# Performance work log

Measured on AMD Instinct MI355X. Metric: run time of the kernel, lower is better.

Reference implementation:

```python
import jax, jax.numpy as jnp
import numpy as np

B, T, N, F_IN = 2, 4, 1024, 256
H, N_HIDDEN = 8, 128
SLOPE = 0.2
NEG_INF = -9e16


def setup_inputs() -> dict:
    key = jax.random.key(0)
    k1, k2, k3, k4 = jax.random.split(key, 4)
    h = jax.random.normal(k1, (B, T, N, F_IN), dtype=jnp.float32)
    adj_mat = jax.random.randint(k2, (N, N), 0, 2, dtype=jnp.int32)
    W = jax.random.normal(k3, (F_IN, H * N_HIDDEN), dtype=jnp.float32) * 0.05
    a = jax.random.normal(k4, (H, 2 * N_HIDDEN, 1), dtype=jnp.float32) * 0.05
    return {"h": h, "adj_mat": adj_mat, "W": W, "a": a}


def reference(h, adj_mat, W, a):
    b, t, n, _ = h.shape
    # linear transform: [B,T,N,F_in] @ [F_in, H*nh] -> [B,T,N,H*nh]
    ht = jnp.einsum('btjs,sh->btjh', h, W)
    # dropout is identity in eval mode
    ht = ht.reshape(b, t, n, H, N_HIDDEN).transpose(0, 1, 3, 2, 4)  # [B,T,H,N,nh]
    # additive attention scores
    a_src = a[:, :N_HIDDEN, :]   # [H, nh, 1]
    a_tgt = a[:, N_HIDDEN:, :]   # [H, nh, 1]
    src = jnp.einsum('bthnd,hdo->bthno', ht, a_src)  # [B,T,H,N,1]
    tgt = jnp.einsum('bthnd,hdo->bthno', ht, a_tgt)  # [B,T,H,N,1]
    e = src + jnp.swapaxes(tgt, -1, -2)              # [B,T,H,N,N]
    e = jnp.where(e >= 0, e, SLOPE * e)              # LeakyReLU
    e = jnp.where(adj_mat > 0, e, jnp.float32(NEG_INF))
    attention = jax.nn.softmax(e, axis=-1)
    # weighted aggregation: [B,T,H,N,N] @ [B,T,H,N,nh]
    h_prime = jnp.einsum('bthij,bthjd->bthid', attention, ht)
    # concat=False branch: mean over dim 0 (batch), as in the source
    return h_prime.mean(axis=0)  # [T,H,N,nh]
```

## Files before the change

kernel.cpp:

```cpp
#include <hip/hip_runtime.h>
#include <cstddef>
#include <cstdint>

#define B_ 2
#define T_ 4
#define N_ 1024
#define FIN_ 256
#define H_ 8
#define D_ 128
#define L2E_ 1.4426950408889634f

typedef __attribute__((ext_vector_type(8))) short short8;
typedef __attribute__((ext_vector_type(4))) float f32x4;
typedef __attribute__((ext_vector_type(2))) float f32x2;

#define MFMA16(A, B, C) __builtin_amdgcn_mfma_f32_16x16x32_bf16((A), (B), (C), 0, 0, 0)

__device__ __forceinline__ unsigned short f2bf(float f) {
    uint32_t u = __float_as_uint(f);
    uint32_t r = (u + 0x7fffu + ((u >> 16) & 1u)) >> 16;
    return (unsigned short)r;
}

__device__ __forceinline__ uint32_t cvt_pk_bf16(float lo, float hi) {
    uint32_t r;
    asm volatile("v_cvt_pk_bf16_f32 %0, %1, %2" : "=v"(r) : "v"(lo), "v"(hi));
    return r;
}

__device__ __forceinline__ float fexp2(float x) {
#if __has_builtin(__builtin_amdgcn_exp2f)
    return __builtin_amdgcn_exp2f(x);
#else
    float r;
    asm("v_exp_f32 %0, %1" : "=v"(r) : "v"(x));
    return r;
#endif
}

__device__ __forceinline__ void load_lds16(const unsigned short* g, unsigned short* l) {
    __builtin_amdgcn_global_load_lds(
        (const __attribute__((address_space(1))) uint32_t*)g,
        (__attribute__((address_space(3))) uint32_t*)l, 16, 0, 0);
}

__global__ __launch_bounds__(256) void k_prep(const int* __restrict__ adj,
                                              const float* __restrict__ W,
                                              const float* __restrict__ a,
                                              unsigned short* __restrict__ Wt_bf,
                                              uint32_t* __restrict__ adjm,
                                              float* __restrict__ wa) {
    __shared__ float wl[64][68];
    const int bid = blockIdx.x, tid = threadIdx.x;
    if (bid < 512) {
        const int w0 = (bid * 256 + tid) * 4;
        const int4 p0 = *(const int4*)(adj + (size_t)w0 * 2);
        const int4 p1 = *(const int4*)(adj + (size_t)w0 * 2 + 4);
        uint4 m;
        m.x = (p0.x > 0 ? 0xFFFFu : 0u) | (p0.y > 0 ? 0xFFFF0000u : 0u);
        m.y = (p0.z > 0 ? 0xFFFFu : 0u) | (p0.w > 0 ? 0xFFFF0000u : 0u);
        m.z = (p1.x > 0 ? 0xFFFFu : 0u) | (p1.y > 0 ? 0xFFFF0000u : 0u);
        m.w = (p1.z > 0 ? 0xFFFFu : 0u) | (p1.w > 0 ? 0xFFFF0000u : 0u);
        *(uint4*)(adjm + w0) = m;
    } else if (bid < 576) {
        const int tb  = bid - 512;
        const int hk0 = (tb >> 2) * 64;
        const int s0  = (tb & 3) * 64;
        {
            const int r  = tid >> 2;
            const int c0 = (tid & 3) * 16;
            #pragma unroll
            for (int k = 0; k < 4; ++k)
                *(float4*)&wl[r][c0 + k * 4] =
                    *(const float4*)(W + (size_t)(s0 + r) * (H_ * D_) + hk0 + c0 + k * 4);
        }
        __syncthreads();
        {
            const int r2 = tid >> 2;
            const int c2 = (tid & 3) * 16;
            unsigned short ob[16];
            #pragma unroll
            for (int k = 0; k < 16; ++k) ob[k] = f2bf(wl[c2 + k][r2]);
            unsigned short* dst = Wt_bf + (size_t)(hk0 + r2) * FIN_ + s0 + c2;
            *(uint4*)(dst)     = *(uint4*)&ob[0];
            *(uint4*)(dst + 8) = *(uint4*)&ob[8];
        }
    } else {
        const int o    = (bid - 576) * 256 + tid;
        const int head = o >> 9;
        const int st   = (o >> 8) & 1;
        const int s    = o & 255;
        const float* wr = W + (size_t)s * (H_ * D_) + head * D_;
        const float* ar = a + head * 256 + st * 128;
        float sum = 0.f;
        #pragma unroll
        for (int d = 0; d < 128; d += 4) {
            const float4 wv = *(const float4*)(wr + d);
            const float4 av = *(const float4*)(ar + d);
            sum += wv.x * av.x + wv.y * av.y + wv.z * av.z + wv.w * av.w;
        }
        wa[s * 16 + head * 2 + st] = sum;
    }
}

__global__ __launch_bounds__(256, 2) void k_gemm_sp(const float* __restrict__ h,
                                                    const unsigned short* __restrict__ Wt_bf,
                                                    const float* __restrict__ wa,
                                                    unsigned short* __restrict__ htT,
                                                    float* __restrict__ s1,
                                                    float* __restrict__ t1) {
    __shared__ __align__(16) char smem[24576];
    const int bid = blockIdx.x, tid = threadIdx.x;
    if (bid < 1024) {
        unsigned short* a_lds = (unsigned short*)smem;
        unsigned short* b_lds = (unsigned short*)(smem + 16384);
        const int xcd  = bid & 7;
        const int slot = bid >> 3;
        const int gid  = xcd * 8 + (slot >> 4);
        const int bt   = gid >> 3;
        const int n0   = (gid & 7) * 128;
        const int hk0  = (slot & 15) * 64;
        const int w = tid >> 6, lane = tid & 63;
        const int row16 = lane & 15, kgrp = lane >> 4;
        const int kswz = (kgrp ^ ((row16 >> 1) & 3)) * 8;
        const int ar  = tid >> 1;
        const int akh = tid & 1;
        const int asub = ar >> 4, arow = ar & 15;
        const int ax = (arow >> 1) & 3;
        const int aslot0 = ((akh * 2) ^ ax) * 8;
        const int aslot1 = ((akh * 2 + 1) ^ ax) * 8;
        const float* ga = h + ((size_t)bt * N_ + n0 + ar) * FIN_ + akh * 16;
        unsigned short* aw_ = a_lds + asub * 512 + arow * 32;
        const int brow = lane >> 2;
        const int bsb  = (lane & 3) ^ ((lane >> 3) & 3);
        const unsigned short* gb = Wt_bf + (size_t)(hk0 + w * 16 + brow) * FIN_ + bsb * 8;
        unsigned short* bw_ = b_lds + w * 512 + (size_t)lane * 8;

        float4 rf0, rf1, rf2, rf3;

#define LOADA(KS) {                                                            \
        const float* g = ga + (KS) * 32;                                       \
        rf0 = *(const float4*)(g);      rf1 = *(const float4*)(g + 4);         \
        rf2 = *(const float4*)(g + 8);  rf3 = *(const float4*)(g + 12); }

#define WRITEA(BUF) {                                                          \
        uint4 o0, o1;                                                          \
        o0.x = cvt_pk_bf16(rf0.x, rf0.y); o0.y = cvt_pk_bf16(rf0.z, rf0.w);    \
        o0.z = cvt_pk_bf16(rf1.x, rf1.y); o0.w = cvt_pk_bf16(rf1.z, rf1.w);    \
        o1.x = cvt_pk_bf16(rf2.x, rf2.y); o1.y = cvt_pk_bf16(rf2.z, rf2.w);    \
        o1.z = cvt_pk_bf16(rf3.x, rf3.y); o1.w = cvt_pk_bf16(rf3.z, rf3.w);    \
        unsigned short* ad = aw_ + (BUF) * 4096;                               \
        *(uint4*)(ad + aslot0) = o0;                                           \
        *(uint4*)(ad + aslot1) = o1; }

#define COMPK(BUF) {                                                           \
        const unsigned short* ab = a_lds + (BUF) * 4096;                       \
        const short8 bfv = *(const short8*)(b_lds + (BUF) * 2048 + w * 512 + row16 * 32 + kswz); \
        _Pragma("unroll")                                                      \
        for (int nt = 0; nt < 8; ++nt) {                                       \
            const short8 afv = *(const short8*)(ab + nt * 512 + row16 * 32 + kswz); \
            acc[nt] = MFMA16(afv, bfv, acc[nt]);                               \
        } }

        f32x4 acc[8];
        #pragma unroll
        for (int nt = 0; nt < 8; ++nt) acc[nt] = (f32x4){0.f, 0.f, 0.f, 0.f};

        LOADA(0)
        WRITEA(0)
        load_lds16(gb, bw_);
        LOADA(1)
        asm volatile("s_waitcnt vmcnt(4) lgkmcnt(0)" ::: "memory");
        __builtin_amdgcn_s_barrier();

        for (int ks = 0; ks < 8; ++ks) {
            const int cur = ks & 1;
            WRITEA(cur ^ 1)
            load_lds16(gb + ((ks + 1) & 7) * 32, bw_ + (cur ^ 1) * 2048);
            LOADA((ks + 2) & 7)
            COMPK(cur)
            asm volatile("s_waitcnt vmcnt(4) lgkmcnt(0)" ::: "memory");
            __builtin_amdgcn_s_barrier();
        }
#undef LOADA
#undef WRITEA
#undef COMPK
        const int hk   = hk0 + w * 16 + row16;
        const int head = hk >> 7;
        const int d    = hk & 127;
        unsigned short* ob = htT + ((size_t)(bt * H_ + head) * D_ + d) * N_;
        #pragma unroll
        for (int nt = 0; nt < 8; ++nt) {
            ushort4 v;
            v.x = f2bf(acc[nt][0]); v.y = f2bf(acc[nt][1]);
            v.z = f2bf(acc[nt][2]); v.w = f2bf(acc[nt][3]);
            *(ushort4*)(ob + n0 + nt * 16 + kgrp * 4) = v;
        }
    } else {
        float (*was)[16] = (float(*)[16])smem;
        {
            const int f = tid * 16;
            #pragma unroll
            for (int k = 0; k < 4; ++k)
                *(float4*)&was[f >> 4][k * 4] = *(const float4*)(wa + f + k * 4);
        }
        __syncthreads();
        const int r = tid >> 2, q = tid & 3;
        const int R = (bid - 1024) * 64 + r;
        const float* hrow = h + (size_t)R * FIN_ + q * 64;
        float acc[16];
        #pragma unroll
        for (int o = 0; o < 16; ++o) acc[o] = 0.f;
        for (int k = 0; k < 64; k += 4) {
            const float4 hv = *(const float4*)(hrow + k);
            const int s = q * 64 + k;
            #pragma unroll
            for (int kk = 0; kk < 4; ++kk) {
                const float hs = (kk == 0) ? hv.x : (kk == 1) ? hv.y : (kk == 2) ? hv.z : hv.w;
                #pragma unroll
                for (int o = 0; o < 16; ++o) acc[o] += hs * was[s + kk][o];
            }
        }
        #pragma unroll
        for (int o = 0; o < 16; ++o) {
            acc[o] += __shfl_xor(acc[o], 1);
            acc[o] += __shfl_xor(acc[o], 2);
        }
        const int bt = R >> 10, n = R & 1023;
        #pragma unroll
        for (int k = 0; k < 4; ++k) {
            const int o = q * 4 + k;
            const int head = o >> 1;
            const size_t idx = ((size_t)(bt * H_ + head)) * N_ + n;
            const float v = acc[o] * L2E_;
            if (o & 1) t1[idx] = v;
            else       s1[idx] = v;
        }
    }
}

struct SC {
    float4 a1l, a1h;
    uint4  m4A, m4B;
};

__global__ __launch_bounds__(256, 2) void k_attn(const unsigned short* __restrict__ htT,
                                                 const float* __restrict__ s1,
                                                 const float* __restrict__ t1,
                                                 const uint32_t* __restrict__ adjm,
                                                 float* __restrict__ out) {
    __shared__ __align__(16) char smem[65536];
    unsigned short* stg = (unsigned short*)smem;
    const int xcd  = blockIdx.x & 7;
    const int slot = blockIdx.x >> 3;
    const int th   = xcd * 4 + (slot >> 4);
    const int i0   = (slot & 15) * 64;
    const int tid = threadIdx.x;
    const int w = tid >> 6, lane = tid & 63;
    const int b = w & 1, isub = w >> 1;
    const int row16 = lane & 15, kgrp = lane >> 4, jrel = kgrp * 8;
    const int kswz = (kgrp ^ ((row16 >> 1) & 3)) * 8;
    const int bth = b * (T_ * H_) + th;
    const int iA  = i0 + isub * 32 + row16;
    const int iB  = iA + 16;
    const float s1A = s1[(size_t)bth * N_ + iA];
    const float s1B = s1[(size_t)bth * N_ + iB];
    const f32x2 s1A2 = {s1A, s1A}, s1B2 = {s1B, s1B};
    const f32x2 c02  = {0.2f, 0.2f};
    const float* t1b = t1 + (size_t)bth * N_;
    const uint32_t* amA = adjm + (size_t)iA * (N_ / 2);
    const uint32_t* amB = adjm + (size_t)iB * (N_ / 2);

    const int sb  = w >> 1;
    const int sd0 = (w & 1) * 64 + (lane >> 2);
    const int sj  = ((lane & 3) ^ ((lane >> 3) & 3)) * 8;
    const unsigned short* gstg = htT + ((size_t)(sb * (T_ * H_) + th) * D_ + sd0) * N_ + sj;
    unsigned short* lstg = stg + (size_t)w * 2048 + (size_t)lane * 8;

#define STAGE(BUF, T32) {                                        \
        const unsigned short* gs = gstg + (size_t)(T32) * 32;    \
        unsigned short* ls = lstg + (BUF) * 8192;                \
        load_lds16(gs,           ls);                            \
        load_lds16(gs + 16 * N_, ls + 512);                      \
        load_lds16(gs + 32 * N_, ls + 1024);                     \
        load_lds16(gs + 48 * N_, ls + 1536); }

#define LOADSC(S, T32) {                                         \
        S.a1l = *(const float4*)(t1b + (T32) * 32 + jrel);       \
        S.a1h = *(const float4*)(t1b + (T32) * 32 + jrel + 4);   \
        S.m4A = *(const uint4*)(amA + (T32) * 16 + kgrp * 4);    \
        S.m4B = *(const uint4*)(amB + (T32) * 16 + kgrp * 4); }

    f32x4 accA[8], accB[8];
    #pragma unroll
    for (int nt = 0; nt < 8; ++nt) {
        accA[nt] = (f32x4){0.f, 0.f, 0.f, 0.f};
        accB[nt] = (f32x4){0.f, 0.f, 0.f, 0.f};
    }
    f32x4 daccA = (f32x4){0.f, 0.f, 0.f, 0.f};
    f32x4 daccB = (f32x4){0.f, 0.f, 0.f, 0.f};
    short8 ones8;
    {
        const short ov = (row16 == 0) ? (short)0x3F80 : (short)0;
        #pragma unroll
        for (int e = 0; e < 8; ++e) ones8[e] = ov;
    }
    const unsigned short* rdbase = stg + b * 4096 + row16 * 32 + kswz;

    SC scA, scB;

#define SUBP(BUFIDX, SCS, TNEXT)                                               \
    {                                                                          \
        const f32x2 tq[4] = {{SCS.a1l.x, SCS.a1l.y}, {SCS.a1l.z, SCS.a1l.w},   \
                             {SCS.a1h.x, SCS.a1h.y}, {SCS.a1h.z, SCS.a1h.w}};  \
        const uint32_t mAw[4] = {SCS.m4A.x, SCS.m4A.y, SCS.m4A.z, SCS.m4A.w};  \
        const uint32_t mBw[4] = {SCS.m4B.x, SCS.m4B.y, SCS.m4B.z, SCS.m4B.w};  \
        short8 afA, afB;                                                       \
        _Pragma("unroll")                                                      \
        for (int p = 0; p < 4; ++p) {                                          \
            const f32x2 eA  = s1A2 + tq[p];                                    \
            const f32x2 eB  = s1B2 + tq[p];                                    \
            const f32x2 eA2 = eA * c02;                                        \
            const f32x2 eB2 = eB * c02;                                        \
            const float wA0 = fexp2(fmaxf(eA[0], eA2[0]));                     \
            const float wA1 = fexp2(fmaxf(eA[1], eA2[1]));                     \
            const float wB0 = fexp2(fmaxf(eB[0], eB2[0]));                     \
            const float wB1 = fexp2(fmaxf(eB[1], eB2[1]));                     \
            ((uint32_t*)&afA)[p] = cvt_pk_bf16(wA0, wA1) & mAw[p];             \
            ((uint32_t*)&afB)[p] = cvt_pk_bf16(wB0, wB1) & mBw[p];             \
        }                                                                      \
        LOADSC(SCS, (TNEXT))                                                   \
        const unsigned short* rb = rdbase + (BUFIDX) * 8192;                   \
        short8 bfr[8];                                                         \
        _Pragma("unroll")                                                      \
        for (int nt = 0; nt < 8; ++nt) bfr[nt] = *(const short8*)(rb + nt * 512); \
        _Pragma("unroll")                                                      \
        for (int nt = 0; nt < 8; ++nt) {                                       \
            accA[nt] = MFMA16(afA, bfr[nt], accA[nt]);                         \
            accB[nt] = MFMA16(afB, bfr[nt], accB[nt]);                         \
        }                                                                      \
        daccA = MFMA16(afA, ones8, daccA);                                     \
        daccB = MFMA16(afB, ones8, daccB);                                     \
    }

    STAGE(0, 0)
    STAGE(1, 1)
    LOADSC(scA, 0)
    LOADSC(scB, 1)

    for (int T = 0; T < 16; ++T) {
        const int pair  = T & 1;
        const int npair = pair ^ 1;
        asm volatile("s_waitcnt vmcnt(8)" ::: "memory");
        __builtin_amdgcn_s_barrier();
        asm volatile("" ::: "memory");
        STAGE(npair * 2,     (2 * T + 2) & 31)
        STAGE(npair * 2 + 1, (2 * T + 3) & 31)
        SUBP(pair * 2,     scA, (2 * T + 2) & 31)
        SUBP(pair * 2 + 1, scB, (2 * T + 3) & 31)
    }
#undef SUBP
#undef LOADSC
#undef STAGE

    __syncthreads();

    float ivA[4], ivB[4];
    #pragma unroll
    for (int r = 0; r < 4; ++r) {
        ivA[r] = __shfl(1.0f / daccA[r], kgrp * 16);
        ivB[r] = __shfl(1.0f / daccB[r], kgrp * 16);
    }

    float* comb = (float*)smem;
    if (b == 1) {
        #pragma unroll
        for (int nt = 0; nt < 8; ++nt)
            #pragma unroll
            for (int r = 0; r < 4; ++r) {
                const int il = isub * 32 + kgrp * 4 + r;
                const int d  = nt * 16 + row16;
                comb[il * 128 + d]        = accA[nt][r] * ivA[r];
                comb[(il + 16) * 128 + d] = accB[nt][r] * ivB[r];
            }
    }
    __syncthreads();
    if (b == 0) {
        #pragma unroll
        for (int nt = 0; nt < 8; ++nt)
            #pragma unroll
            for (int r = 0; r < 4; ++r) {
                const int il = isub * 32 + kgrp * 4 + r;
                const int d  = nt * 16 + row16;
                out[((size_t)th * N_ + i0 + il) * D_ + d] =
                    0.5f * (accA[nt][r] * ivA[r] + comb[il * 128 + d]);
                out[((size_t)th * N_ + i0 + il + 16) * D_ + d] =
                    0.5f * (accB[nt][r] * ivB[r] + comb[(il + 16) * 128 + d]);
            }
    }
}

extern "C" void kernel_launch(void* const* d_in, const int* in_sizes, int n_in,
                              void* d_out, int out_size, void* d_ws, size_t ws_size,
                              hipStream_t stream) {
    const float* h   = (const float*)d_in[0];
    const int*   adj = (const int*)d_in[1];
    const float* W   = (const float*)d_in[2];
    const float* a   = (const float*)d_in[3];
    float* out = (float*)d_out;

    char* p = (char*)d_ws;
    unsigned short* htT = (unsigned short*)p;  p += (size_t)B_ * T_ * H_ * D_ * N_ * 2;
    float* s1 = (float*)p;                     p += (size_t)B_ * T_ * H_ * N_ * 4;
    float* t1 = (float*)p;                     p += (size_t)B_ * T_ * H_ * N_ * 4;
    uint32_t* adjm = (uint32_t*)p;             p += (size_t)N_ * N_ / 2 * 4;
    unsigned short* Wt_bf = (unsigned short*)p;p += (size_t)(H_ * D_) * FIN_ * 2;
    float* wa = (float*)p;

    k_prep<<<dim3(592), dim3(256), 0, stream>>>(adj, W, a, Wt_bf, adjm, wa);
    k_gemm_sp<<<dim3(1152), dim3(256), 0, stream>>>(h, Wt_bf, wa, htT, s1, t1);
    k_attn<<<dim3(512), dim3(256), 0, stream>>>(htT, s1, t1, adjm, out);
}
```

Measured before the change: 73.20 us.

## Move adjacency mask packing into GEMM kernel and make attention staging per-wave

```diff
diff --git a/kernel.cpp b/kernel.cpp
--- a/kernel.cpp
+++ b/kernel.cpp
@@ -44,26 +44,14 @@
         (__attribute__((address_space(3))) uint32_t*)l, 16, 0, 0);
 }
 
-__global__ __launch_bounds__(256) void k_prep(const int* __restrict__ adj,
-                                              const float* __restrict__ W,
+__global__ __launch_bounds__(256) void k_prep(const float* __restrict__ W,
                                               const float* __restrict__ a,
                                               unsigned short* __restrict__ Wt_bf,
-                                              uint32_t* __restrict__ adjm,
                                               float* __restrict__ wa) {
     __shared__ float wl[64][68];
     const int bid = blockIdx.x, tid = threadIdx.x;
-    if (bid < 512) {
-        const int w0 = (bid * 256 + tid) * 4;
-        const int4 p0 = *(const int4*)(adj + (size_t)w0 * 2);
-        const int4 p1 = *(const int4*)(adj + (size_t)w0 * 2 + 4);
-        uint4 m;
-        m.x = (p0.x > 0 ? 0xFFFFu : 0u) | (p0.y > 0 ? 0xFFFF0000u : 0u);
-        m.y = (p0.z > 0 ? 0xFFFFu : 0u) | (p0.w > 0 ? 0xFFFF0000u : 0u);
-        m.z = (p1.x > 0 ? 0xFFFFu : 0u) | (p1.y > 0 ? 0xFFFF0000u : 0u);
-        m.w = (p1.z > 0 ? 0xFFFFu : 0u) | (p1.w > 0 ? 0xFFFF0000u : 0u);
-        *(uint4*)(adjm + w0) = m;
-    } else if (bid < 576) {
-        const int tb  = bid - 512;
+    if (bid < 64) {
+        const int tb  = bid;
         const int hk0 = (tb >> 2) * 64;
         const int s0  = (tb & 3) * 64;
         {
@@ -86,7 +74,7 @@
             *(uint4*)(dst + 8) = *(uint4*)&ob[8];
         }
     } else {
-        const int o    = (bid - 576) * 256 + tid;
+        const int o    = (bid - 64) * 256 + tid;
         const int head = o >> 9;
         const int st   = (o >> 8) & 1;
         const int s    = o & 255;
@@ -106,9 +94,11 @@
 __global__ __launch_bounds__(256, 2) void k_gemm_sp(const float* __restrict__ h,
                                                     const unsigned short* __restrict__ Wt_bf,
                                                     const float* __restrict__ wa,
+                                                    const int* __restrict__ adj,
                                                     unsigned short* __restrict__ htT,
                                                     float* __restrict__ s1,
-                                                    float* __restrict__ t1) {
+                                                    float* __restrict__ t1,
+                                                    uint32_t* __restrict__ adjm) {
     __shared__ __align__(16) char smem[24576];
     const int bid = blockIdx.x, tid = threadIdx.x;
     if (bid < 1024) {
@@ -196,7 +186,7 @@
             v.z = f2bf(acc[nt][2]); v.w = f2bf(acc[nt][3]);
             *(ushort4*)(ob + n0 + nt * 16 + kgrp * 4) = v;
         }
-    } else {
+    } else if (bid < 1152) {
         float (*was)[16] = (float(*)[16])smem;
         {
             const int f = tid * 16;
@@ -236,6 +226,16 @@
             if (o & 1) t1[idx] = v;
             else       s1[idx] = v;
         }
+    } else {
+        const int w0 = ((bid - 1152) * 256 + tid) * 4;
+        const int4 p0 = *(const int4*)(adj + (size_t)w0 * 2);
+        const int4 p1 = *(const int4*)(adj + (size_t)w0 * 2 + 4);
+        uint4 m;
+        m.x = (p0.x > 0 ? 0xFFFFu : 0u) | (p0.y > 0 ? 0xFFFF0000u : 0u);
+        m.y = (p0.z > 0 ? 0xFFFFu : 0u) | (p0.w > 0 ? 0xFFFF0000u : 0u);
+        m.z = (p1.x > 0 ? 0xFFFFu : 0u) | (p1.y > 0 ? 0xFFFF0000u : 0u);
+        m.w = (p1.z > 0 ? 0xFFFFu : 0u) | (p1.w > 0 ? 0xFFFF0000u : 0u);
+        *(uint4*)(adjm + w0) = m;
     }
 }
 
@@ -271,19 +271,22 @@
     const uint32_t* amA = adjm + (size_t)iA * (N_ / 2);
     const uint32_t* amB = adjm + (size_t)iB * (N_ / 2);
 
-    const int sb  = w >> 1;
-    const int sd0 = (w & 1) * 64 + (lane >> 2);
-    const int sj  = ((lane & 3) ^ ((lane >> 3) & 3)) * 8;
-    const unsigned short* gstg = htT + ((size_t)(sb * (T_ * H_) + th) * D_ + sd0) * N_ + sj;
-    unsigned short* lstg = stg + (size_t)w * 2048 + (size_t)lane * 8;
+    const int sd0 = lane >> 2;
+    const int sj  = ((lane & 3) ^ ((sd0 >> 1) & 3)) * 8;
+    const unsigned short* gstg = htT + ((size_t)bth * D_ + sd0) * N_ + sj;
+    unsigned short* lstg = stg + (size_t)w * 8192 + (size_t)lane * 8;
 
 #define STAGE(BUF, T32) {                                        \
         const unsigned short* gs = gstg + (size_t)(T32) * 32;    \
-        unsigned short* ls = lstg + (BUF) * 8192;                \
-        load_lds16(gs,           ls);                            \
-        load_lds16(gs + 16 * N_, ls + 512);                      \
-        load_lds16(gs + 32 * N_, ls + 1024);                     \
-        load_lds16(gs + 48 * N_, ls + 1536); }
+        unsigned short* ls = lstg + (BUF) * 4096;                \
+        load_lds16(gs,            ls);                           \
+        load_lds16(gs + 16 * N_,  ls + 512);                     \
+        load_lds16(gs + 32 * N_,  ls + 1024);                    \
+        load_lds16(gs + 48 * N_,  ls + 1536);                    \
+        load_lds16(gs + 64 * N_,  ls + 2048);                    \
+        load_lds16(gs + 80 * N_,  ls + 2560);                    \
+        load_lds16(gs + 96 * N_,  ls + 3072);                    \
+        load_lds16(gs + 112 * N_, ls + 3584); }
 
 #define LOADSC(S, T32) {                                         \
         S.a1l = *(const float4*)(t1b + (T32) * 32 + jrel);       \
@@ -305,16 +308,16 @@
         #pragma unroll
         for (int e = 0; e < 8; ++e) ones8[e] = ov;
     }
-    const unsigned short* rdbase = stg + b * 4096 + row16 * 32 + kswz;
-
-    SC scA, scB;
-
-#define SUBP(BUFIDX, SCS, TNEXT)                                               \
+    const unsigned short* rdbase = stg + (size_t)w * 8192 + row16 * 32 + kswz;
+
+    SC sc;
+
+#define SUBP(BUFIDX, TNEXT)                                                    \
     {                                                                          \
-        const f32x2 tq[4] = {{SCS.a1l.x, SCS.a1l.y}, {SCS.a1l.z, SCS.a1l.w},   \
-                             {SCS.a1h.x, SCS.a1h.y}, {SCS.a1h.z, SCS.a1h.w}};  \
-        const uint32_t mAw[4] = {SCS.m4A.x, SCS.m4A.y, SCS.m4A.z, SCS.m4A.w};  \
-        const uint32_t mBw[4] = {SCS.m4B.x, SCS.m4B.y, SCS.m4B.z, SCS.m4B.w};  \
+        const f32x2 tq[4] = {{sc.a1l.x, sc.a1l.y}, {sc.a1l.z, sc.a1l.w},       \
+                             {sc.a1h.x, sc.a1h.y}, {sc.a1h.z, sc.a1h.w}};      \
+        const uint32_t mAw[4] = {sc.m4A.x, sc.m4A.y, sc.m4A.z, sc.m4A.w};      \
+        const uint32_t mBw[4] = {sc.m4B.x, sc.m4B.y, sc.m4B.z, sc.m4B.w};      \
         short8 afA, afB;                                                       \
         _Pragma("unroll")                                                      \
         for (int p = 0; p < 4; ++p) {                                          \
@@ -329,8 +332,8 @@
             ((uint32_t*)&afA)[p] = cvt_pk_bf16(wA0, wA1) & mAw[p];             \
             ((uint32_t*)&afB)[p] = cvt_pk_bf16(wB0, wB1) & mBw[p];             \
         }                                                                      \
-        LOADSC(SCS, (TNEXT))                                                   \
-        const unsigned short* rb = rdbase + (BUFIDX) * 8192;                   \
+        LOADSC(sc, (TNEXT))                                                    \
+        const unsigned short* rb = rdbase + (BUFIDX) * 4096;                   \
         short8 bfr[8];                                                         \
         _Pragma("unroll")                                                      \
         for (int nt = 0; nt < 8; ++nt) bfr[nt] = *(const short8*)(rb + nt * 512); \
@@ -344,26 +347,16 @@
     }
 
     STAGE(0, 0)
-    STAGE(1, 1)
-    LOADSC(scA, 0)
-    LOADSC(scB, 1)
-
-    for (int T = 0; T < 16; ++T) {
-        const int pair  = T & 1;
-        const int npair = pair ^ 1;
-        asm volatile("s_waitcnt vmcnt(8)" ::: "memory");
-        __builtin_amdgcn_s_barrier();
-        asm volatile("" ::: "memory");
-        STAGE(npair * 2,     (2 * T + 2) & 31)
-        STAGE(npair * 2 + 1, (2 * T + 3) & 31)
-        SUBP(pair * 2,     scA, (2 * T + 2) & 31)
-        SUBP(pair * 2 + 1, scB, (2 * T + 3) & 31)
+    LOADSC(sc, 0)
+
+    for (int t = 0; t < 32; ++t) {
+        STAGE((t + 1) & 1, (t + 1) & 31)
+        asm volatile("s_waitcnt vmcnt(12)" ::: "memory");
+        SUBP(t & 1, (t + 1) & 31)
     }
 #undef SUBP
 #undef LOADSC
 #undef STAGE
-
-    __syncthreads();
 
     float ivA[4], ivB[4];
     #pragma unroll
@@ -372,6 +365,7 @@
         ivB[r] = __shfl(1.0f / daccB[r], kgrp * 16);
     }
 
+    __syncthreads();
     float* comb = (float*)smem;
     if (b == 1) {
         #pragma unroll
@@ -417,7 +411,7 @@
     unsigned short* Wt_bf = (unsigned short*)p;p += (size_t)(H_ * D_) * FIN_ * 2;
     float* wa = (float*)p;
 
-    k_prep<<<dim3(592), dim3(256), 0, stream>>>(adj, W, a, Wt_bf, adjm, wa);
-    k_gemm_sp<<<dim3(1152), dim3(256), 0, stream>>>(h, Wt_bf, wa, htT, s1, t1);
+    k_prep<<<dim3(80), dim3(256), 0, stream>>>(W, a, Wt_bf, wa);
+    k_gemm_sp<<<dim3(1664), dim3(256), 0, stream>>>(h, Wt_bf, wa, adj, htT, s1, t1, adjm);
     k_attn<<<dim3(512), dim3(256), 0, stream>>>(htT, s1, t1, adjm, out);
 }
```

After: 78.86 us. 7.7% more time.
